# Kernel tuning notes

Hardware: AMD Instinct MI355X
Metric: run time of the kernel (lower is better)

## Reference

```python
import jax, jax.numpy as jnp
import numpy as np
import math

SR = 96000.0
FRAME = 2048
NB = 16
GAIN_RANGE = (-24.0, 24.0)
Q_RANGE = (0.5, 16.0)
BROADBAND = (-60.0, 0.0)
HPF_R = (20.0, 500.0)
LPF_R = (5000.0, 20000.0)
SHELF_R = (50.0, 16000.0)
PEAK_R = (100.0, 15000.0)


def _dfreq(n, rng):
    lo, hi = math.log(rng[0]), math.log(rng[1])
    return jnp.exp(lo + n * (hi - lo))


def _dgain(n, rng=GAIN_RANGE):
    return rng[0] + n * (rng[1] - rng[0])


def _dq(n):
    lo, hi = math.log(Q_RANGE[0]), math.log(Q_RANGE[1])
    return jnp.exp(lo + n * (hi - lo))


def _coeffs(ftype, fc, gain_db, Q):
    # returns stacked [g, k, a1, a2, a3, m0, m1, m2], each same shape as fc
    g = jnp.clip(jnp.tan(math.pi * fc / SR), 1e-6, 100.0)
    Q = jnp.clip(Q, 0.1, 100.0)
    one = jnp.ones_like(g)
    zero = jnp.zeros_like(g)
    if ftype in ('highpass', 'lowpass'):
        k = 1.0 / Q
        a1 = 1.0 / (1.0 + g * (g + k)); a2 = g * a1; a3 = g * a2
        if ftype == 'highpass':
            m0, m1, m2 = one, -k, -one
        else:
            m0, m1, m2 = zero, zero, one
    elif ftype == 'peak':
        A = jnp.power(10.0, gain_db / 40.0)
        k = jnp.where(gain_db >= 0, 1.0 / (Q * A), A / Q)
        a1 = 1.0 / (1.0 + g * (g + k)); a2 = g * a1; a3 = g * a2
        m0, m1, m2 = one, k * (A * A - 1.0), zero
    elif ftype == 'lowshelf':
        A = jnp.power(10.0, gain_db / 40.0); sA = jnp.sqrt(A); k = 1.0 / Q
        gs = jnp.where(gain_db >= 0, g / sA, g * sA)
        a1 = 1.0 / (1.0 + gs * (gs + k)); a2 = gs * a1; a3 = gs * a2
        m0, m1, m2 = one, k * (A - 1.0), A * A - 1.0
    else:  # highshelf
        A = jnp.power(10.0, gain_db / 40.0); sA = jnp.sqrt(A); k = 1.0 / Q
        gs = jnp.where(gain_db >= 0, g * sA, g / sA)
        a1 = 1.0 / (1.0 + gs * (gs + k)); a2 = gs * a1; a3 = gs * a2
        m0, m1, m2 = A * A, k * (1.0 - A) * A, 1.0 - A * A
    return jnp.stack([g, k, a1, a2, a3, m0, m1, m2], 0)


def _all_coeffs(params, n_frames_audio):
    # params: (B, 50, n_frames_params) -> coeffs (nF, NB, 8, B), in/out gains (nF, B)
    B = params.shape[0]
    nFp = params.shape[2]
    pidx = jnp.minimum(jnp.arange(n_frames_audio), nFp - 1)
    fp = jnp.take(params, pidx, axis=2)                 # (B, 50, nF)
    bq = fp[:, :NB * 3, :].reshape(B, NB, 3, n_frames_audio)
    in_g = jnp.power(10.0, _dgain(fp[:, -2, :], BROADBAND) / 20.0)   # (B, nF)
    out_g = jnp.power(10.0, _dgain(fp[:, -1, :], BROADBAND) / 20.0)  # (B, nF)
    cs = []
    for i in range(NB):
        fn, gn, qn = bq[:, i, 0], bq[:, i, 1], bq[:, i, 2]  # (B, nF)
        Q = _dq(qn)
        if i == 0:
            c = _coeffs('highpass', _dfreq(fn, HPF_R), None, Q)
        elif i == 15:
            c = _coeffs('lowpass', _dfreq(fn, LPF_R), None, Q)
        elif i == 1:
            c = _coeffs('lowshelf', _dfreq(fn, SHELF_R), _dgain(gn), Q)
        elif i == 14:
            c = _coeffs('highshelf', _dfreq(fn, SHELF_R), _dgain(gn), Q)
        else:
            c = _coeffs('peak', _dfreq(fn, PEAK_R), _dgain(gn), Q)
        cs.append(c)  # (8, B, nF)
    coeffs = jnp.transpose(jnp.stack(cs, 0), (3, 0, 1, 2))  # (nF, NB, 8, B)
    return coeffs, in_g.T, out_g.T


def _forward(audio, params):
    B, S = audio.shape
    nF = S // FRAME  # S chosen as exact multiple of FRAME
    coeffs, in_g, out_g = _all_coeffs(params, nF)
    frames = jnp.transpose(audio.reshape(B, nF, FRAME), (1, 2, 0))  # (nF, FRAME, B)

    def frame_step(states, xs):
        fr, c, ig, og = xs  # fr (FRAME,B), c (NB,8,B), ig (B,), og (B,)
        x = fr * ig[None, :]
        new_states = []
        for i in range(NB):
            a1, a2, a3 = c[i, 2], c[i, 3], c[i, 4]
            m0, m1, m2 = c[i, 5], c[i, 6], c[i, 7]

            def samp(st, xn, a1=a1, a2=a2, a3=a3, m0=m0, m1=m1, m2=m2):
                ic1, ic2 = st
                v3 = xn - ic2
                v1 = a1 * ic1 + a2 * v3
                v2 = ic2 + a2 * v1 + a3 * v3
                out = m0 * xn + m1 * v1 + m2 * v2
                return (2.0 * v1 - ic1, 2.0 * v2 - ic2), out

            (ic1, ic2), x = jax.lax.scan(samp, (states[i, 0], states[i, 1]), x)
            new_states.append(jnp.stack([ic1, ic2], 0))
        return jnp.stack(new_states, 0), x * og[None, :]

    init = jnp.zeros((NB, 2, B), audio.dtype)
    _, out = jax.lax.scan(frame_step, init, (frames, coeffs, in_g, out_g))
    return jnp.transpose(out, (2, 0, 1)).reshape(B, S)  # (B, S)


_forward_jit = jax.jit(_forward)


def setup_inputs() -> dict:
    key = jax.random.key(0)
    k1, k2 = jax.random.split(key)
    B, S, nFp = 32, 49152, 24  # 24 frames of 2048 samples
    audio = jax.random.normal(k1, (B, S), dtype=jnp.float32) * 0.1
    params = jax.random.uniform(k2, (B, 50, nFp), dtype=jnp.float32)
    return {'audio': audio, 'params': params}


def reference(audio, params):
    return _forward_jit(audio, params)
```

## Files before the change

kernel.cpp:

```cpp
#include <hip/hip_runtime.h>
#include <math.h>

#define NBATCH 32
#define S      49152
#define NF     24
#define NB     16
#define NBLK   4
#define CHUNK  16
#define NCH    768
#define NWAVE  12

__device__ __forceinline__ float clampf(float x, float lo, float hi) {
    return fminf(fmaxf(x, lo), hi);
}

#define FOREACH_S(OP) \
    OP(s00) OP(s01) OP(s02) OP(s03) OP(s04) OP(s05) OP(s06) OP(s07) \
    OP(s08) OP(s09) OP(s10) OP(s11) OP(s12) OP(s13) OP(s14) OP(s15)

#define DECL_S(x) float x;

#define STEPA(x) { \
    const float n1_ = fmaf(t00, ic1, fmaf(t01, ic2, b0 * (x))); \
    const float n2_ = fmaf(t10, ic1, fmaf(t11, ic2, b1 * (x))); \
    ic1 = n1_; ic2 = n2_; }

#define STEPC(x) { \
    const float y_  = fmaf(c0, ic1, fmaf(c1, ic2, c2 * (x))); \
    const float n1_ = fmaf(t00, ic1, fmaf(t01, ic2, b0 * (x))); \
    const float n2_ = fmaf(t10, ic1, fmaf(t11, ic2, b1 * (x))); \
    (x) = y_; ic1 = n1_; ic2 = n2_; }

__global__ __launch_bounds__(NCH, 3)
void biquad_chain_kernel(const float* __restrict__ audio,
                         const float* __restrict__ params,
                         float* __restrict__ out,
                         unsigned int* __restrict__ ws)
{
    __shared__ float sc[NB][NF][16];
    __shared__ float sgain[2][NF];
    __shared__ float4 saggM[NWAVE];
    __shared__ float  saggC[NWAVE][2];
    __shared__ float  sv[NWAVE][2];

    const int t       = threadIdx.x;
    const int xcd     = blockIdx.x & 7;
    const int slot_   = blockIdx.x >> 3;
    const int bt      = xcd * 4 + (slot_ & 3);
    const int quarter = slot_ >> 2;
    const int lane    = t & 63;
    const int wave    = t >> 6;
    const int frame   = quarter * 6 + (wave >> 1);

    if (t < NB * NF) {
        const int f  = t / NF;
        const int fr = t % NF;
        const float* P = params + (size_t)bt * 50 * NF;
        const float fn = P[(3 * f + 0) * NF + fr];
        const float gn = P[(3 * f + 1) * NF + fr];
        const float qn = P[(3 * f + 2) * NF + fr];

        float Q = __expf(-0.69314718f + qn * 3.4657359f);
        Q = clampf(Q, 0.1f, 100.0f);

        float lo, hi;
        int type;
        if      (f == 0)  { lo = 20.0f;   hi = 500.0f;   type = 0; }
        else if (f == 15) { lo = 5000.0f; hi = 20000.0f; type = 1; }
        else if (f == 1)  { lo = 50.0f;   hi = 16000.0f; type = 3; }
        else if (f == 14) { lo = 50.0f;   hi = 16000.0f; type = 4; }
        else              { lo = 100.0f;  hi = 15000.0f; type = 2; }

        const float fc = __expf(__logf(lo) + fn * (__logf(hi) - __logf(lo)));
        float g_ = __tanf((float)M_PI * fc / 96000.0f);
        g_ = clampf(g_, 1e-6f, 100.0f);
        const float gdb = -24.0f + 48.0f * gn;

        float a1, a2, a3, m0, m1, m2;
        if (type == 0 || type == 1) {
            const float k = 1.0f / Q;
            a1 = 1.0f / (1.0f + g_ * (g_ + k)); a2 = g_ * a1; a3 = g_ * a2;
            if (type == 0) { m0 = 1.0f; m1 = -k;   m2 = -1.0f; }
            else           { m0 = 0.0f; m1 = 0.0f; m2 = 1.0f;  }
        } else if (type == 2) {
            const float A = __expf(gdb * (2.30258509f / 40.0f));
            const float k = (gdb >= 0.0f) ? 1.0f / (Q * A) : A / Q;
            a1 = 1.0f / (1.0f + g_ * (g_ + k)); a2 = g_ * a1; a3 = g_ * a2;
            m0 = 1.0f; m1 = k * (A * A - 1.0f); m2 = 0.0f;
        } else {
            const float A  = __expf(gdb * (2.30258509f / 40.0f));
            const float sA = sqrtf(A);
            const float k  = 1.0f / Q;
            float gs;
            if (type == 3) gs = (gdb >= 0.0f) ? g_ / sA : g_ * sA;
            else           gs = (gdb >= 0.0f) ? g_ * sA : g_ / sA;
            a1 = 1.0f / (1.0f + gs * (gs + k)); a2 = gs * a1; a3 = gs * a2;
            if (type == 3) { m0 = 1.0f;  m1 = k * (A - 1.0f);      m2 = A * A - 1.0f; }
            else           { m0 = A * A; m1 = k * (1.0f - A) * A;  m2 = 1.0f - A * A; }
        }

        const float q2  = a2 * a2 + a3;
        const float t00 = 2.0f * a1 - 1.0f;
        const float t01 = -2.0f * a2;
        const float t10 = 2.0f * a1 * a2;
        const float t11 = 1.0f - 2.0f * q2;
        const float b0  = 2.0f * a2;
        const float b1  = 2.0f * q2;
        const float c0  = a1 * (m1 + m2 * a2);
        const float c1  = m2 * (1.0f - q2) - m1 * a2;
        const float c2  = m0 + m1 * a2 + m2 * q2;

        float u00 = t00, u01 = t01, u10 = t10, u11 = t11;
        #pragma unroll
        for (int i = 0; i < 4; i++) {
            const float n00 = u00 * u00 + u01 * u10;
            const float n01 = u00 * u01 + u01 * u11;
            const float n10 = u10 * u00 + u11 * u10;
            const float n11 = u10 * u01 + u11 * u11;
            u00 = n00; u01 = n01; u10 = n10; u11 = n11;
        }

        sc[f][fr][0] = t00; sc[f][fr][1] = t01; sc[f][fr][2] = t10; sc[f][fr][3] = t11;
        sc[f][fr][4] = b0;  sc[f][fr][5] = b1;  sc[f][fr][6] = c0;  sc[f][fr][7] = c1;
        sc[f][fr][8] = c2;  sc[f][fr][9] = u00; sc[f][fr][10] = u01; sc[f][fr][11] = u10;
        sc[f][fr][12] = u11;
    }
    if (t >= 384 && t < 384 + 2 * NF) {
        const int idx = t - 384;
        const int which = idx / NF;
        const int fr    = idx % NF;
        const float* P = params + (size_t)bt * 50 * NF;
        const float p  = P[(48 + which) * NF + fr];
        const float db = -60.0f + 60.0f * p;
        sgain[which][fr] = __expf(db * (2.30258509f / 20.0f));
    }
    __syncthreads();

    FOREACH_S(DECL_S)
    {
        const float ing = sgain[0][frame];
        const float* base = audio + (size_t)bt * S
                          + (size_t)(quarter * NCH + t) * CHUNK;
        float4 q;
        q = *(const float4*)(base +  0); s00 = q.x*ing; s01 = q.y*ing; s02 = q.z*ing; s03 = q.w*ing;
        q = *(const float4*)(base +  4); s04 = q.x*ing; s05 = q.y*ing; s06 = q.z*ing; s07 = q.w*ing;
        q = *(const float4*)(base +  8); s08 = q.x*ing; s09 = q.y*ing; s10 = q.z*ing; s11 = q.w*ing;
        q = *(const float4*)(base + 12); s12 = q.x*ing; s13 = q.y*ing; s14 = q.z*ing; s15 = q.w*ing;
    }

    #pragma unroll 1
    for (int f = 0; f < NB; f++) {
        const float4 q0 = *(const float4*)&sc[f][frame][0];
        const float4 q1 = *(const float4*)&sc[f][frame][4];
        const float4 q2 = *(const float4*)&sc[f][frame][8];
        const float  M11v = sc[f][frame][12];
        const float t00 = q0.x, t01 = q0.y, t10 = q0.z, t11 = q0.w;
        const float b0  = q1.x, b1  = q1.y, c0  = q1.z, c1  = q1.w;
        const float c2  = q2.x;

        float ic1 = 0.0f, ic2 = 0.0f;
        FOREACH_S(STEPA)

        float Md00 = q2.y, Md01 = q2.z, Md10 = q2.w, Md11 = M11v;
        float Ac0 = ic1, Ac1 = ic2;
        #pragma unroll
        for (int d = 1; d < 64; d <<= 1) {
            const float lc0 = __shfl_up(Ac0, d);
            const float lc1 = __shfl_up(Ac1, d);
            if (lane >= d) {
                Ac0 = fmaf(Md00, lc0, fmaf(Md01, lc1, Ac0));
                Ac1 = fmaf(Md10, lc0, fmaf(Md11, lc1, Ac1));
            }
            const float n00 = Md00 * Md00 + Md01 * Md10;
            const float n01 = Md00 * Md01 + Md01 * Md11;
            const float n10 = Md10 * Md00 + Md11 * Md10;
            const float n11 = Md10 * Md01 + Md11 * Md11;
            Md00 = n00; Md01 = n01; Md10 = n10; Md11 = n11;
        }

        if (lane == 63) {
            saggM[wave] = make_float4(Md00, Md01, Md10, Md11);
            saggC[wave][0] = Ac0; saggC[wave][1] = Ac1;
        }
        __syncthreads();

        const unsigned int tag = (unsigned int)(f + 1);
        unsigned int* stagebase = ws + ((bt * NB + f) * NBLK) * 8;

        if (wave == 0) {
            float G00 = 1.0f, G01 = 0.0f, G10 = 0.0f, G11 = 1.0f, Gc0 = 0.0f, Gc1 = 0.0f;
            if (lane < NWAVE) {
                const float4 m = saggM[lane];
                G00 = m.x; G01 = m.y; G10 = m.z; G11 = m.w;
                Gc0 = saggC[lane][0]; Gc1 = saggC[lane][1];
            }
            #pragma unroll
            for (int d = 1; d < 16; d <<= 1) {
                const float l00 = __shfl_up(G00, d);
                const float l01 = __shfl_up(G01, d);
                const float l10 = __shfl_up(G10, d);
                const float l11 = __shfl_up(G11, d);
                const float lc0 = __shfl_up(Gc0, d);
                const float lc1 = __shfl_up(Gc1, d);
                if (lane >= d && lane < NWAVE) {
                    const float n00 = G00 * l00 + G01 * l10;
                    const float n01 = G00 * l01 + G01 * l11;
                    const float n10 = G10 * l00 + G11 * l10;
                    const float n11 = G10 * l01 + G11 * l11;
                    const float nc0 = G00 * lc0 + G01 * lc1 + Gc0;
                    const float nc1 = G10 * lc0 + G11 * lc1 + Gc1;
                    G00 = n00; G01 = n01; G10 = n10; G11 = n11;
                    Gc0 = nc0; Gc1 = nc1;
                }
            }

            if (quarter < NBLK - 1 && lane == NWAVE - 1) {
                unsigned int* slot = stagebase + quarter * 8;
                float* dp = (float*)(slot + 1);
                __hip_atomic_store(&dp[0], G00, __ATOMIC_RELAXED, __HIP_MEMORY_SCOPE_AGENT);
                __hip_atomic_store(&dp[1], G01, __ATOMIC_RELAXED, __HIP_MEMORY_SCOPE_AGENT);
                __hip_atomic_store(&dp[2], G10, __ATOMIC_RELAXED, __HIP_MEMORY_SCOPE_AGENT);
                __hip_atomic_store(&dp[3], G11, __ATOMIC_RELAXED, __HIP_MEMORY_SCOPE_AGENT);
                __hip_atomic_store(&dp[4], Gc0, __ATOMIC_RELAXED, __HIP_MEMORY_SCOPE_AGENT);
                __hip_atomic_store(&dp[5], Gc1, __ATOMIC_RELAXED, __HIP_MEMORY_SCOPE_AGENT);
                __hip_atomic_store(slot, tag, __ATOMIC_RELEASE, __HIP_MEMORY_SCOPE_AGENT);
            }

            float P00 = __shfl_up(G00, 1);
            float P01 = __shfl_up(G01, 1);
            float P10 = __shfl_up(G10, 1);
            float P11 = __shfl_up(G11, 1);
            float Pc0 = __shfl_up(Gc0, 1);
            float Pc1 = __shfl_up(Gc1, 1);
            if (lane == 0) { P00 = 1.0f; P01 = 0.0f; P10 = 0.0f; P11 = 1.0f; Pc0 = 0.0f; Pc1 = 0.0f; }

            float S0x = 0.0f, S0y = 0.0f;
            if (lane == 0 && quarter > 0) {
                float sx = 0.0f, sy = 0.0f;
                for (int k2 = 0; k2 < quarter; k2++) {
                    unsigned int* slot = stagebase + k2 * 8;
                    while (__hip_atomic_load(slot, __ATOMIC_ACQUIRE, __HIP_MEMORY_SCOPE_AGENT) != tag) {
                        __builtin_amdgcn_s_sleep(1);
                    }
                    float* dp = (float*)(slot + 1);
                    const float m00 = __hip_atomic_load(&dp[0], __ATOMIC_RELAXED, __HIP_MEMORY_SCOPE_AGENT);
                    const float m01 = __hip_atomic_load(&dp[1], __ATOMIC_RELAXED, __HIP_MEMORY_SCOPE_AGENT);
                    const float m10 = __hip_atomic_load(&dp[2], __ATOMIC_RELAXED, __HIP_MEMORY_SCOPE_AGENT);
                    const float m11 = __hip_atomic_load(&dp[3], __ATOMIC_RELAXED, __HIP_MEMORY_SCOPE_AGENT);
                    const float cc0 = __hip_atomic_load(&dp[4], __ATOMIC_RELAXED, __HIP_MEMORY_SCOPE_AGENT);
                    const float cc1 = __hip_atomic_load(&dp[5], __ATOMIC_RELAXED, __HIP_MEMORY_SCOPE_AGENT);
                    const float nx = m00 * sx + m01 * sy + cc0;
                    const float ny = m10 * sx + m11 * sy + cc1;
                    sx = nx; sy = ny;
                }
                S0x = sx; S0y = sy;
            }
            S0x = __shfl(S0x, 0);
            S0y = __shfl(S0y, 0);

            if (lane < NWAVE) {
                sv[lane][0] = fmaf(P00, S0x, fmaf(P01, S0y, Pc0));
                sv[lane][1] = fmaf(P10, S0x, fmaf(P11, S0y, Pc1));
            }
        }
        __syncthreads();

        const float vx = sv[wave][0];
        const float vy = sv[wave][1];

        float ce0 = __shfl_up(Ac0, 1);
        float ce1 = __shfl_up(Ac1, 1);
        if (lane == 0) { ce0 = 0.0f; ce1 = 0.0f; }

        float w0 = vx, w1 = vy;
        float p00 = q2.y, p01 = q2.z, p10 = q2.w, p11 = M11v;
        #pragma unroll
        for (int b = 0; b < 6; b++) {
            if (lane & (1 << b)) {
                const float nw0 = fmaf(p00, w0, p01 * w1);
                const float nw1 = fmaf(p10, w0, p11 * w1);
                w0 = nw0; w1 = nw1;
            }
            if (b < 5) {
                const float n00 = p00 * p00 + p01 * p10;
                const float n01 = p00 * p01 + p01 * p11;
                const float n10 = p10 * p00 + p11 * p10;
                const float n11 = p10 * p01 + p11 * p11;
                p00 = n00; p01 = n01; p10 = n10; p11 = n11;
            }
        }
        ic1 = w0 + ce0;
        ic2 = w1 + ce1;

        FOREACH_S(STEPC)
    }

    {
        const float og = sgain[1][frame];
        float* base = out + (size_t)bt * S + (size_t)(quarter * NCH + t) * CHUNK;
        float4 q;
        q.x = s00*og; q.y = s01*og; q.z = s02*og; q.w = s03*og; *(float4*)(base +  0) = q;
        q.x = s04*og; q.y = s05*og; q.z = s06*og; q.w = s07*og; *(float4*)(base +  4) = q;
        q.x = s08*og; q.y = s09*og; q.z = s10*og; q.w = s11*og; *(float4*)(base +  8) = q;
        q.x = s12*og; q.y = s13*og; q.z = s14*og; q.w = s15*og; *(float4*)(base + 12) = q;
    }
}

extern "C" void kernel_launch(void* const* d_in, const int* in_sizes, int n_in,
                              void* d_out, int out_size, void* d_ws, size_t ws_size,
                              hipStream_t stream)
{
    const float* audio  = (const float*)d_in[0];
    const float* params = (const float*)d_in[1];
    float* out = (float*)d_out;
    unsigned int* ws = (unsigned int*)d_ws;
    biquad_chain_kernel<<<NBLK * NBATCH, NCH, 0, stream>>>(audio, params, out, ws);
}
```

Measured before the change: 125.3 us.

## Replace per-stage block barriers with chained wave-level lookback prefix propagation

The per-filter-stage pair of __syncthreads and the wave-0 combine of wave aggregates are removed. Each wave now spins on an LDS tag from the previous wave (or, for wave 0, a global tag from the previous block). It folds that inclusive prefix into its own aggregate and publishes its inclusive result for the next wave or block. This removes block-wide barriers so waves can move on to later filter stages independently. In exchange, prefix propagation becomes a serial chain across all waves and blocks, and it relies on spin-waiting with s_sleep.

Measured after the change: 123.1 us. No clear change (-1.8%).

```diff
diff --git a/kernel.cpp b/kernel.cpp
--- a/kernel.cpp
+++ b/kernel.cpp
@@ -39,9 +39,8 @@
 {
     __shared__ float sc[NB][NF][16];
     __shared__ float sgain[2][NF];
-    __shared__ float4 saggM[NWAVE];
-    __shared__ float  saggC[NWAVE][2];
-    __shared__ float  sv[NWAVE][2];
+    __shared__ float4 sincl[NB][NWAVE][2];
+    __shared__ unsigned int stag[NB][NWAVE];
 
     const int t       = threadIdx.x;
     const int xcd     = blockIdx.x & 7;
@@ -134,6 +133,7 @@
         const float db = -60.0f + 60.0f * p;
         sgain[which][fr] = __expf(db * (2.30258509f / 20.0f));
     }
+    if (t < NB * NWAVE) stag[t / NWAVE][t % NWAVE] = 0u;
     __syncthreads();
 
     FOREACH_S(DECL_S)
@@ -178,101 +178,61 @@
             Md00 = n00; Md01 = n01; Md10 = n10; Md11 = n11;
         }
 
-        if (lane == 63) {
-            saggM[wave] = make_float4(Md00, Md01, Md10, Md11);
-            saggC[wave][0] = Ac0; saggC[wave][1] = Ac1;
-        }
-        __syncthreads();
-
-        const unsigned int tag = (unsigned int)(f + 1);
-        unsigned int* stagebase = ws + ((bt * NB + f) * NBLK) * 8;
-
-        if (wave == 0) {
-            float G00 = 1.0f, G01 = 0.0f, G10 = 0.0f, G11 = 1.0f, Gc0 = 0.0f, Gc1 = 0.0f;
-            if (lane < NWAVE) {
-                const float4 m = saggM[lane];
-                G00 = m.x; G01 = m.y; G10 = m.z; G11 = m.w;
-                Gc0 = saggC[lane][0]; Gc1 = saggC[lane][1];
-            }
-            #pragma unroll
-            for (int d = 1; d < 16; d <<= 1) {
-                const float l00 = __shfl_up(G00, d);
-                const float l01 = __shfl_up(G01, d);
-                const float l10 = __shfl_up(G10, d);
-                const float l11 = __shfl_up(G11, d);
-                const float lc0 = __shfl_up(Gc0, d);
-                const float lc1 = __shfl_up(Gc1, d);
-                if (lane >= d && lane < NWAVE) {
-                    const float n00 = G00 * l00 + G01 * l10;
-                    const float n01 = G00 * l01 + G01 * l11;
-                    const float n10 = G10 * l00 + G11 * l10;
-                    const float n11 = G10 * l01 + G11 * l11;
-                    const float nc0 = G00 * lc0 + G01 * lc1 + Gc0;
-                    const float nc1 = G10 * lc0 + G11 * lc1 + Gc1;
-                    G00 = n00; G01 = n01; G10 = n10; G11 = n11;
-                    Gc0 = nc0; Gc1 = nc1;
-                }
-            }
-
-            if (quarter < NBLK - 1 && lane == NWAVE - 1) {
-                unsigned int* slot = stagebase + quarter * 8;
-                float* dp = (float*)(slot + 1);
-                __hip_atomic_store(&dp[0], G00, __ATOMIC_RELAXED, __HIP_MEMORY_SCOPE_AGENT);
-                __hip_atomic_store(&dp[1], G01, __ATOMIC_RELAXED, __HIP_MEMORY_SCOPE_AGENT);
-                __hip_atomic_store(&dp[2], G10, __ATOMIC_RELAXED, __HIP_MEMORY_SCOPE_AGENT);
-                __hip_atomic_store(&dp[3], G11, __ATOMIC_RELAXED, __HIP_MEMORY_SCOPE_AGENT);
-                __hip_atomic_store(&dp[4], Gc0, __ATOMIC_RELAXED, __HIP_MEMORY_SCOPE_AGENT);
-                __hip_atomic_store(&dp[5], Gc1, __ATOMIC_RELAXED, __HIP_MEMORY_SCOPE_AGENT);
-                __hip_atomic_store(slot, tag, __ATOMIC_RELEASE, __HIP_MEMORY_SCOPE_AGENT);
-            }
-
-            float P00 = __shfl_up(G00, 1);
-            float P01 = __shfl_up(G01, 1);
-            float P10 = __shfl_up(G10, 1);
-            float P11 = __shfl_up(G11, 1);
-            float Pc0 = __shfl_up(Gc0, 1);
-            float Pc1 = __shfl_up(Gc1, 1);
-            if (lane == 0) { P00 = 1.0f; P01 = 0.0f; P10 = 0.0f; P11 = 1.0f; Pc0 = 0.0f; Pc1 = 0.0f; }
-
-            float S0x = 0.0f, S0y = 0.0f;
-            if (lane == 0 && quarter > 0) {
-                float sx = 0.0f, sy = 0.0f;
-                for (int k2 = 0; k2 < quarter; k2++) {
-                    unsigned int* slot = stagebase + k2 * 8;
-                    while (__hip_atomic_load(slot, __ATOMIC_ACQUIRE, __HIP_MEMORY_SCOPE_AGENT) != tag) {
-                        __builtin_amdgcn_s_sleep(1);
-                    }
-                    float* dp = (float*)(slot + 1);
-                    const float m00 = __hip_atomic_load(&dp[0], __ATOMIC_RELAXED, __HIP_MEMORY_SCOPE_AGENT);
-                    const float m01 = __hip_atomic_load(&dp[1], __ATOMIC_RELAXED, __HIP_MEMORY_SCOPE_AGENT);
-                    const float m10 = __hip_atomic_load(&dp[2], __ATOMIC_RELAXED, __HIP_MEMORY_SCOPE_AGENT);
-                    const float m11 = __hip_atomic_load(&dp[3], __ATOMIC_RELAXED, __HIP_MEMORY_SCOPE_AGENT);
-                    const float cc0 = __hip_atomic_load(&dp[4], __ATOMIC_RELAXED, __HIP_MEMORY_SCOPE_AGENT);
-                    const float cc1 = __hip_atomic_load(&dp[5], __ATOMIC_RELAXED, __HIP_MEMORY_SCOPE_AGENT);
-                    const float nx = m00 * sx + m01 * sy + cc0;
-                    const float ny = m10 * sx + m11 * sy + cc1;
-                    sx = nx; sy = ny;
-                }
-                S0x = sx; S0y = sy;
-            }
-            S0x = __shfl(S0x, 0);
-            S0y = __shfl(S0y, 0);
-
-            if (lane < NWAVE) {
-                sv[lane][0] = fmaf(P00, S0x, fmaf(P01, S0y, Pc0));
-                sv[lane][1] = fmaf(P10, S0x, fmaf(P11, S0y, Pc1));
-            }
-        }
-        __syncthreads();
-
-        const float vx = sv[wave][0];
-        const float vy = sv[wave][1];
-
         float ce0 = __shfl_up(Ac0, 1);
         float ce1 = __shfl_up(Ac1, 1);
         if (lane == 0) { ce0 = 0.0f; ce1 = 0.0f; }
 
-        float w0 = vx, w1 = vy;
+        const unsigned int tag = (unsigned int)(f + 1);
+        float Mp00 = 1.0f, Mp01 = 0.0f, Mp10 = 0.0f, Mp11 = 1.0f;
+        float cp0 = 0.0f, cp1 = 0.0f;
+        if (wave > 0) {
+            while (__hip_atomic_load(&stag[f][wave - 1], __ATOMIC_ACQUIRE,
+                                     __HIP_MEMORY_SCOPE_WORKGROUP) != tag)
+                __builtin_amdgcn_s_sleep(1);
+            const float4 d0 = sincl[f][wave - 1][0];
+            const float4 d1 = sincl[f][wave - 1][1];
+            Mp00 = d0.x; Mp01 = d0.y; Mp10 = d0.z; Mp11 = d0.w;
+            cp0 = d1.x; cp1 = d1.y;
+        } else if (quarter > 0) {
+            unsigned int* gs = ws + ((size_t)(bt * NB + f) * NBLK + (quarter - 1)) * 8;
+            while (__hip_atomic_load(gs, __ATOMIC_ACQUIRE,
+                                     __HIP_MEMORY_SCOPE_AGENT) != tag)
+                __builtin_amdgcn_s_sleep(1);
+            const float* dp = (const float*)(gs + 1);
+            Mp00 = __hip_atomic_load(&dp[0], __ATOMIC_RELAXED, __HIP_MEMORY_SCOPE_AGENT);
+            Mp01 = __hip_atomic_load(&dp[1], __ATOMIC_RELAXED, __HIP_MEMORY_SCOPE_AGENT);
+            Mp10 = __hip_atomic_load(&dp[2], __ATOMIC_RELAXED, __HIP_MEMORY_SCOPE_AGENT);
+            Mp11 = __hip_atomic_load(&dp[3], __ATOMIC_RELAXED, __HIP_MEMORY_SCOPE_AGENT);
+            cp0  = __hip_atomic_load(&dp[4], __ATOMIC_RELAXED, __HIP_MEMORY_SCOPE_AGENT);
+            cp1  = __hip_atomic_load(&dp[5], __ATOMIC_RELAXED, __HIP_MEMORY_SCOPE_AGENT);
+        }
+
+        if (lane == 63) {
+            const float I00 = fmaf(Md00, Mp00, Md01 * Mp10);
+            const float I01 = fmaf(Md00, Mp01, Md01 * Mp11);
+            const float I10 = fmaf(Md10, Mp00, Md11 * Mp10);
+            const float I11 = fmaf(Md10, Mp01, Md11 * Mp11);
+            const float Ic0 = fmaf(Md00, cp0, fmaf(Md01, cp1, Ac0));
+            const float Ic1 = fmaf(Md10, cp0, fmaf(Md11, cp1, Ac1));
+            if (wave < NWAVE - 1) {
+                sincl[f][wave][0] = make_float4(I00, I01, I10, I11);
+                sincl[f][wave][1] = make_float4(Ic0, Ic1, 0.0f, 0.0f);
+                __hip_atomic_store(&stag[f][wave], tag, __ATOMIC_RELEASE,
+                                   __HIP_MEMORY_SCOPE_WORKGROUP);
+            } else if (quarter < NBLK - 1) {
+                unsigned int* gs = ws + ((size_t)(bt * NB + f) * NBLK + quarter) * 8;
+                float* dp = (float*)(gs + 1);
+                __hip_atomic_store(&dp[0], I00, __ATOMIC_RELAXED, __HIP_MEMORY_SCOPE_AGENT);
+                __hip_atomic_store(&dp[1], I01, __ATOMIC_RELAXED, __HIP_MEMORY_SCOPE_AGENT);
+                __hip_atomic_store(&dp[2], I10, __ATOMIC_RELAXED, __HIP_MEMORY_SCOPE_AGENT);
+                __hip_atomic_store(&dp[3], I11, __ATOMIC_RELAXED, __HIP_MEMORY_SCOPE_AGENT);
+                __hip_atomic_store(&dp[4], Ic0, __ATOMIC_RELAXED, __HIP_MEMORY_SCOPE_AGENT);
+                __hip_atomic_store(&dp[5], Ic1, __ATOMIC_RELAXED, __HIP_MEMORY_SCOPE_AGENT);
+                __hip_atomic_store(gs, tag, __ATOMIC_RELEASE, __HIP_MEMORY_SCOPE_AGENT);
+            }
+        }
+
+        float w0 = cp0, w1 = cp1;
         float p00 = q2.y, p01 = q2.z, p10 = q2.w, p11 = M11v;
         #pragma unroll
         for (int b = 0; b < 6; b++) {
```

## Split each batch row across eight blocks and scan predecessor carries in parallel

Applied to the files above, without the earlier changes.

Each batch row is now split across eight blocks of eight samples per thread instead of four blocks of sixteen. This doubles the grid to 256 blocks and halves the serial per-thread recurrence length per band. Inter-block carry propagation changes from a serial loop in one lane to a parallel wave-shuffle scan over the predecessor blocks' affine transforms. The cost is more cross-block spin-wait synchronization per band and more scan overhead relative to per-thread work. It also relies on all 256 blocks being co-resident.

Result: slower. 146.9 us (+17.2%).

```diff
diff --git a/kernel.cpp b/kernel.cpp
--- a/kernel.cpp
+++ b/kernel.cpp
@@ -5,8 +5,8 @@
 #define S      49152
 #define NF     24
 #define NB     16
-#define NBLK   4
-#define CHUNK  16
+#define NBLK   8
+#define CHUNK  8
 #define NCH    768
 #define NWAVE  12
 
@@ -15,8 +15,7 @@
 }
 
 #define FOREACH_S(OP) \
-    OP(s00) OP(s01) OP(s02) OP(s03) OP(s04) OP(s05) OP(s06) OP(s07) \
-    OP(s08) OP(s09) OP(s10) OP(s11) OP(s12) OP(s13) OP(s14) OP(s15)
+    OP(s00) OP(s01) OP(s02) OP(s03) OP(s04) OP(s05) OP(s06) OP(s07)
 
 #define DECL_S(x) float x;
 
@@ -44,13 +43,11 @@
     __shared__ float  sv[NWAVE][2];
 
     const int t       = threadIdx.x;
-    const int xcd     = blockIdx.x & 7;
-    const int slot_   = blockIdx.x >> 3;
-    const int bt      = xcd * 4 + (slot_ & 3);
-    const int quarter = slot_ >> 2;
+    const int bt      = blockIdx.x & 31;
+    const int oct     = blockIdx.x >> 5;
     const int lane    = t & 63;
     const int wave    = t >> 6;
-    const int frame   = quarter * 6 + (wave >> 1);
+    const int frame   = oct * 3 + (wave >> 2);
 
     if (t < NB * NF) {
         const int f  = t / NF;
@@ -112,7 +109,7 @@
 
         float u00 = t00, u01 = t01, u10 = t10, u11 = t11;
         #pragma unroll
-        for (int i = 0; i < 4; i++) {
+        for (int i = 0; i < 3; i++) {
             const float n00 = u00 * u00 + u01 * u10;
             const float n01 = u00 * u01 + u01 * u11;
             const float n10 = u10 * u00 + u11 * u10;
@@ -140,12 +137,10 @@
     {
         const float ing = sgain[0][frame];
         const float* base = audio + (size_t)bt * S
-                          + (size_t)(quarter * NCH + t) * CHUNK;
+                          + (size_t)(oct * NCH + t) * CHUNK;
         float4 q;
-        q = *(const float4*)(base +  0); s00 = q.x*ing; s01 = q.y*ing; s02 = q.z*ing; s03 = q.w*ing;
-        q = *(const float4*)(base +  4); s04 = q.x*ing; s05 = q.y*ing; s06 = q.z*ing; s07 = q.w*ing;
-        q = *(const float4*)(base +  8); s08 = q.x*ing; s09 = q.y*ing; s10 = q.z*ing; s11 = q.w*ing;
-        q = *(const float4*)(base + 12); s12 = q.x*ing; s13 = q.y*ing; s14 = q.z*ing; s15 = q.w*ing;
+        q = *(const float4*)(base + 0); s00 = q.x*ing; s01 = q.y*ing; s02 = q.z*ing; s03 = q.w*ing;
+        q = *(const float4*)(base + 4); s04 = q.x*ing; s05 = q.y*ing; s06 = q.z*ing; s07 = q.w*ing;
     }
 
     #pragma unroll 1
@@ -185,7 +180,7 @@
         __syncthreads();
 
         const unsigned int tag = (unsigned int)(f + 1);
-        unsigned int* stagebase = ws + ((bt * NB + f) * NBLK) * 8;
+        unsigned int* stagebase = ws + ((size_t)(bt * NB + f) * NBLK) * 8;
 
         if (wave == 0) {
             float G00 = 1.0f, G01 = 0.0f, G10 = 0.0f, G11 = 1.0f, Gc0 = 0.0f, Gc1 = 0.0f;
@@ -214,8 +209,8 @@
                 }
             }
 
-            if (quarter < NBLK - 1 && lane == NWAVE - 1) {
-                unsigned int* slot = stagebase + quarter * 8;
+            if (oct < NBLK - 1 && lane == NWAVE - 1) {
+                unsigned int* slot = stagebase + oct * 8;
                 float* dp = (float*)(slot + 1);
                 __hip_atomic_store(&dp[0], G00, __ATOMIC_RELAXED, __HIP_MEMORY_SCOPE_AGENT);
                 __hip_atomic_store(&dp[1], G01, __ATOMIC_RELAXED, __HIP_MEMORY_SCOPE_AGENT);
@@ -235,28 +230,44 @@
             if (lane == 0) { P00 = 1.0f; P01 = 0.0f; P10 = 0.0f; P11 = 1.0f; Pc0 = 0.0f; Pc1 = 0.0f; }
 
             float S0x = 0.0f, S0y = 0.0f;
-            if (lane == 0 && quarter > 0) {
-                float sx = 0.0f, sy = 0.0f;
-                for (int k2 = 0; k2 < quarter; k2++) {
-                    unsigned int* slot = stagebase + k2 * 8;
+            if (oct > 0) {
+                float A00 = 1.0f, A01 = 0.0f, A10 = 0.0f, A11 = 1.0f;
+                float Acx = 0.0f, Acy = 0.0f;
+                if (lane < oct) {
+                    unsigned int* slot = stagebase + lane * 8;
                     while (__hip_atomic_load(slot, __ATOMIC_ACQUIRE, __HIP_MEMORY_SCOPE_AGENT) != tag) {
                         __builtin_amdgcn_s_sleep(1);
                     }
-                    float* dp = (float*)(slot + 1);
-                    const float m00 = __hip_atomic_load(&dp[0], __ATOMIC_RELAXED, __HIP_MEMORY_SCOPE_AGENT);
-                    const float m01 = __hip_atomic_load(&dp[1], __ATOMIC_RELAXED, __HIP_MEMORY_SCOPE_AGENT);
-                    const float m10 = __hip_atomic_load(&dp[2], __ATOMIC_RELAXED, __HIP_MEMORY_SCOPE_AGENT);
-                    const float m11 = __hip_atomic_load(&dp[3], __ATOMIC_RELAXED, __HIP_MEMORY_SCOPE_AGENT);
-                    const float cc0 = __hip_atomic_load(&dp[4], __ATOMIC_RELAXED, __HIP_MEMORY_SCOPE_AGENT);
-                    const float cc1 = __hip_atomic_load(&dp[5], __ATOMIC_RELAXED, __HIP_MEMORY_SCOPE_AGENT);
-                    const float nx = m00 * sx + m01 * sy + cc0;
-                    const float ny = m10 * sx + m11 * sy + cc1;
-                    sx = nx; sy = ny;
+                    const float* dp = (const float*)(slot + 1);
+                    A00 = __hip_atomic_load(&dp[0], __ATOMIC_RELAXED, __HIP_MEMORY_SCOPE_AGENT);
+                    A01 = __hip_atomic_load(&dp[1], __ATOMIC_RELAXED, __HIP_MEMORY_SCOPE_AGENT);
+                    A10 = __hip_atomic_load(&dp[2], __ATOMIC_RELAXED, __HIP_MEMORY_SCOPE_AGENT);
+                    A11 = __hip_atomic_load(&dp[3], __ATOMIC_RELAXED, __HIP_MEMORY_SCOPE_AGENT);
+                    Acx = __hip_atomic_load(&dp[4], __ATOMIC_RELAXED, __HIP_MEMORY_SCOPE_AGENT);
+                    Acy = __hip_atomic_load(&dp[5], __ATOMIC_RELAXED, __HIP_MEMORY_SCOPE_AGENT);
                 }
-                S0x = sx; S0y = sy;
-            }
-            S0x = __shfl(S0x, 0);
-            S0y = __shfl(S0y, 0);
+                #pragma unroll
+                for (int d = 1; d < 8; d <<= 1) {
+                    const float l00 = __shfl_up(A00, d);
+                    const float l01 = __shfl_up(A01, d);
+                    const float l10 = __shfl_up(A10, d);
+                    const float l11 = __shfl_up(A11, d);
+                    const float lcx = __shfl_up(Acx, d);
+                    const float lcy = __shfl_up(Acy, d);
+                    if (lane >= d && lane < oct) {
+                        const float n00 = A00 * l00 + A01 * l10;
+                        const float n01 = A00 * l01 + A01 * l11;
+                        const float n10 = A10 * l00 + A11 * l10;
+                        const float n11 = A10 * l01 + A11 * l11;
+                        const float ncx = fmaf(A00, lcx, fmaf(A01, lcy, Acx));
+                        const float ncy = fmaf(A10, lcx, fmaf(A11, lcy, Acy));
+                        A00 = n00; A01 = n01; A10 = n10; A11 = n11;
+                        Acx = ncx; Acy = ncy;
+                    }
+                }
+                S0x = __shfl(Acx, oct - 1);
+                S0y = __shfl(Acy, oct - 1);
+            }
 
             if (lane < NWAVE) {
                 sv[lane][0] = fmaf(P00, S0x, fmaf(P01, S0y, Pc0));
@@ -297,12 +308,10 @@
 
     {
         const float og = sgain[1][frame];
-        float* base = out + (size_t)bt * S + (size_t)(quarter * NCH + t) * CHUNK;
+        float* base = out + (size_t)bt * S + (size_t)(oct * NCH + t) * CHUNK;
         float4 q;
-        q.x = s00*og; q.y = s01*og; q.z = s02*og; q.w = s03*og; *(float4*)(base +  0) = q;
-        q.x = s04*og; q.y = s05*og; q.z = s06*og; q.w = s07*og; *(float4*)(base +  4) = q;
-        q.x = s08*og; q.y = s09*og; q.z = s10*og; q.w = s11*og; *(float4*)(base +  8) = q;
-        q.x = s12*og; q.y = s13*og; q.z = s14*og; q.w = s15*og; *(float4*)(base + 12) = q;
+        q.x = s00*og; q.y = s01*og; q.z = s02*og; q.w = s03*og; *(float4*)(base + 0) = q;
+        q.x = s04*og; q.y = s05*og; q.z = s06*og; q.w = s07*og; *(float4*)(base + 4) = q;
     }
 }
 
```

## Split each batch across two blocks with 32-sample chunks per thread

Applied to the files above, without the earlier changes.

Each batch row is now processed by two blocks, each taking half the signal, instead of four blocks taking a quarter each. Every thread handles 32 samples rather than 16, and the chunk transition matrix is raised to the 32nd power. The cross-block handoff is now a single state vector that the first half publishes and the second half waits on, with no chain of affine compositions. This cuts the spin-wait chain and the inter-block synchronization per stage. In exchange each thread runs a longer serial recurrence, there are half as many blocks (64), and register pressure rises.

Measured after the change: 182.8 us. 1.46x slower.

```diff
diff --git a/kernel.cpp b/kernel.cpp
--- a/kernel.cpp
+++ b/kernel.cpp
@@ -5,8 +5,8 @@
 #define S      49152
 #define NF     24
 #define NB     16
-#define NBLK   4
-#define CHUNK  16
+#define NBLK   2
+#define CHUNK  32
 #define NCH    768
 #define NWAVE  12
 
@@ -16,7 +16,9 @@
 
 #define FOREACH_S(OP) \
     OP(s00) OP(s01) OP(s02) OP(s03) OP(s04) OP(s05) OP(s06) OP(s07) \
-    OP(s08) OP(s09) OP(s10) OP(s11) OP(s12) OP(s13) OP(s14) OP(s15)
+    OP(s08) OP(s09) OP(s10) OP(s11) OP(s12) OP(s13) OP(s14) OP(s15) \
+    OP(s16) OP(s17) OP(s18) OP(s19) OP(s20) OP(s21) OP(s22) OP(s23) \
+    OP(s24) OP(s25) OP(s26) OP(s27) OP(s28) OP(s29) OP(s30) OP(s31)
 
 #define DECL_S(x) float x;
 
@@ -44,13 +46,11 @@
     __shared__ float  sv[NWAVE][2];
 
     const int t       = threadIdx.x;
-    const int xcd     = blockIdx.x & 7;
-    const int slot_   = blockIdx.x >> 3;
-    const int bt      = xcd * 4 + (slot_ & 3);
-    const int quarter = slot_ >> 2;
+    const int bt      = blockIdx.x & 31;
+    const int half    = blockIdx.x >> 5;
     const int lane    = t & 63;
     const int wave    = t >> 6;
-    const int frame   = quarter * 6 + (wave >> 1);
+    const int frame   = half * NWAVE + wave;
 
     if (t < NB * NF) {
         const int f  = t / NF;
@@ -112,7 +112,7 @@
 
         float u00 = t00, u01 = t01, u10 = t10, u11 = t11;
         #pragma unroll
-        for (int i = 0; i < 4; i++) {
+        for (int i = 0; i < 5; i++) {
             const float n00 = u00 * u00 + u01 * u10;
             const float n01 = u00 * u01 + u01 * u11;
             const float n10 = u10 * u00 + u11 * u10;
@@ -139,13 +139,17 @@
     FOREACH_S(DECL_S)
     {
         const float ing = sgain[0][frame];
-        const float* base = audio + (size_t)bt * S
-                          + (size_t)(quarter * NCH + t) * CHUNK;
+        const float* base = audio + (size_t)bt * S + (size_t)half * (S / 2)
+                          + (size_t)t * CHUNK;
         float4 q;
         q = *(const float4*)(base +  0); s00 = q.x*ing; s01 = q.y*ing; s02 = q.z*ing; s03 = q.w*ing;
         q = *(const float4*)(base +  4); s04 = q.x*ing; s05 = q.y*ing; s06 = q.z*ing; s07 = q.w*ing;
         q = *(const float4*)(base +  8); s08 = q.x*ing; s09 = q.y*ing; s10 = q.z*ing; s11 = q.w*ing;
         q = *(const float4*)(base + 12); s12 = q.x*ing; s13 = q.y*ing; s14 = q.z*ing; s15 = q.w*ing;
+        q = *(const float4*)(base + 16); s16 = q.x*ing; s17 = q.y*ing; s18 = q.z*ing; s19 = q.w*ing;
+        q = *(const float4*)(base + 20); s20 = q.x*ing; s21 = q.y*ing; s22 = q.z*ing; s23 = q.w*ing;
+        q = *(const float4*)(base + 24); s24 = q.x*ing; s25 = q.y*ing; s26 = q.z*ing; s27 = q.w*ing;
+        q = *(const float4*)(base + 28); s28 = q.x*ing; s29 = q.y*ing; s30 = q.z*ing; s31 = q.w*ing;
     }
 
     #pragma unroll 1
@@ -185,7 +189,7 @@
         __syncthreads();
 
         const unsigned int tag = (unsigned int)(f + 1);
-        unsigned int* stagebase = ws + ((bt * NB + f) * NBLK) * 8;
+        unsigned int* slot = ws + (size_t)(bt * NB + f) * 8;
 
         if (wave == 0) {
             float G00 = 1.0f, G01 = 0.0f, G10 = 0.0f, G11 = 1.0f, Gc0 = 0.0f, Gc1 = 0.0f;
@@ -214,15 +218,10 @@
                 }
             }
 
-            if (quarter < NBLK - 1 && lane == NWAVE - 1) {
-                unsigned int* slot = stagebase + quarter * 8;
+            if (half == 0 && lane == NWAVE - 1) {
                 float* dp = (float*)(slot + 1);
-                __hip_atomic_store(&dp[0], G00, __ATOMIC_RELAXED, __HIP_MEMORY_SCOPE_AGENT);
-                __hip_atomic_store(&dp[1], G01, __ATOMIC_RELAXED, __HIP_MEMORY_SCOPE_AGENT);
-                __hip_atomic_store(&dp[2], G10, __ATOMIC_RELAXED, __HIP_MEMORY_SCOPE_AGENT);
-                __hip_atomic_store(&dp[3], G11, __ATOMIC_RELAXED, __HIP_MEMORY_SCOPE_AGENT);
-                __hip_atomic_store(&dp[4], Gc0, __ATOMIC_RELAXED, __HIP_MEMORY_SCOPE_AGENT);
-                __hip_atomic_store(&dp[5], Gc1, __ATOMIC_RELAXED, __HIP_MEMORY_SCOPE_AGENT);
+                __hip_atomic_store(&dp[0], Gc0, __ATOMIC_RELAXED, __HIP_MEMORY_SCOPE_AGENT);
+                __hip_atomic_store(&dp[1], Gc1, __ATOMIC_RELAXED, __HIP_MEMORY_SCOPE_AGENT);
                 __hip_atomic_store(slot, tag, __ATOMIC_RELEASE, __HIP_MEMORY_SCOPE_AGENT);
             }
 
@@ -235,28 +234,18 @@
             if (lane == 0) { P00 = 1.0f; P01 = 0.0f; P10 = 0.0f; P11 = 1.0f; Pc0 = 0.0f; Pc1 = 0.0f; }
 
             float S0x = 0.0f, S0y = 0.0f;
-            if (lane == 0 && quarter > 0) {
-                float sx = 0.0f, sy = 0.0f;
-                for (int k2 = 0; k2 < quarter; k2++) {
-                    unsigned int* slot = stagebase + k2 * 8;
+            if (half == 1) {
+                if (lane == 0) {
                     while (__hip_atomic_load(slot, __ATOMIC_ACQUIRE, __HIP_MEMORY_SCOPE_AGENT) != tag) {
                         __builtin_amdgcn_s_sleep(1);
                     }
-                    float* dp = (float*)(slot + 1);
-                    const float m00 = __hip_atomic_load(&dp[0], __ATOMIC_RELAXED, __HIP_MEMORY_SCOPE_AGENT);
-                    const float m01 = __hip_atomic_load(&dp[1], __ATOMIC_RELAXED, __HIP_MEMORY_SCOPE_AGENT);
-                    const float m10 = __hip_atomic_load(&dp[2], __ATOMIC_RELAXED, __HIP_MEMORY_SCOPE_AGENT);
-                    const float m11 = __hip_atomic_load(&dp[3], __ATOMIC_RELAXED, __HIP_MEMORY_SCOPE_AGENT);
-                    const float cc0 = __hip_atomic_load(&dp[4], __ATOMIC_RELAXED, __HIP_MEMORY_SCOPE_AGENT);
-                    const float cc1 = __hip_atomic_load(&dp[5], __ATOMIC_RELAXED, __HIP_MEMORY_SCOPE_AGENT);
-                    const float nx = m00 * sx + m01 * sy + cc0;
-                    const float ny = m10 * sx + m11 * sy + cc1;
-                    sx = nx; sy = ny;
+                    const float* dp = (const float*)(slot + 1);
+                    S0x = __hip_atomic_load(&dp[0], __ATOMIC_RELAXED, __HIP_MEMORY_SCOPE_AGENT);
+                    S0y = __hip_atomic_load(&dp[1], __ATOMIC_RELAXED, __HIP_MEMORY_SCOPE_AGENT);
                 }
-                S0x = sx; S0y = sy;
-            }
-            S0x = __shfl(S0x, 0);
-            S0y = __shfl(S0y, 0);
+                S0x = __shfl(S0x, 0);
+                S0y = __shfl(S0y, 0);
+            }
 
             if (lane < NWAVE) {
                 sv[lane][0] = fmaf(P00, S0x, fmaf(P01, S0y, Pc0));
@@ -297,12 +286,17 @@
 
     {
         const float og = sgain[1][frame];
-        float* base = out + (size_t)bt * S + (size_t)(quarter * NCH + t) * CHUNK;
+        float* base = out + (size_t)bt * S + (size_t)half * (S / 2)
+                    + (size_t)t * CHUNK;
         float4 q;
         q.x = s00*og; q.y = s01*og; q.z = s02*og; q.w = s03*og; *(float4*)(base +  0) = q;
         q.x = s04*og; q.y = s05*og; q.z = s06*og; q.w = s07*og; *(float4*)(base +  4) = q;
         q.x = s08*og; q.y = s09*og; q.z = s10*og; q.w = s11*og; *(float4*)(base +  8) = q;
         q.x = s12*og; q.y = s13*og; q.z = s14*og; q.w = s15*og; *(float4*)(base + 12) = q;
+        q.x = s16*og; q.y = s17*og; q.z = s18*og; q.w = s19*og; *(float4*)(base + 16) = q;
+        q.x = s20*og; q.y = s21*og; q.z = s22*og; q.w = s23*og; *(float4*)(base + 20) = q;
+        q.x = s24*og; q.y = s25*og; q.z = s26*og; q.w = s27*og; *(float4*)(base + 24) = q;
+        q.x = s28*og; q.y = s29*og; q.z = s30*og; q.w = s31*og; *(float4*)(base + 28) = q;
     }
 }
 
```
